# Kernel tuning notes

Measured on AMD Instinct MI355X. Metric: run time of the kernel, lower is better.

The kernel has to match this reference:

```python
import jax, jax.numpy as jnp
import numpy as np

B = 4
IN_DIM = 512
HID = 1024
MLP_LAYERS = 2
SEQ = 4096          # output_dim / sequence_length
RH = 64             # ripl_hidden_dim
RL = 2              # ripl_num_layers
MULT = 1            # ripl_coordinate_multipler

MID_DIM = 2 * RH * RH + (RH + 1) * RH      # per middle ripple layer param count
OUT_DIM = 2 * RH * 1 + (RH + 1) * 1        # output ripple layer param count
MLP_OUT = RL * MID_DIM + OUT_DIM


def gelu(x):
    return jax.nn.gelu(x, approximate=False)


def layer_norm(x, g, b, eps=1e-5):
    mu = jnp.mean(x, axis=-1, keepdims=True)
    var = jnp.var(x, axis=-1, keepdims=True)
    return (x - mu) * jax.lax.rsqrt(var + eps) * g + b


def batch_ripple(x, w, b):
    # x: (B,S,I), w: (B,O,I,2), b: (B,O,I+1)
    # out[b,s,o] = b[b,o,0] + sum_i b[b,o,i+1] * sin(w[b,o,i,0]*x[b,s,i] + w[b,o,i,1])
    arg = w[:, None, :, :, 0] * x[:, :, None, :] + w[:, None, :, :, 1]  # (B,S,O,I)
    return b[:, None, :, 0] + jnp.sum(jnp.sin(arg) * b[:, None, :, 1:], axis=-1)


def setup_inputs() -> dict:
    key = jax.random.key(0)
    ks = jax.random.split(key, 20)
    s = 0.02
    inp = {
        "x": jax.random.normal(ks[0], (B, IN_DIM), jnp.float32),
        "mlp_w0": jax.random.normal(ks[1], (IN_DIM, HID), jnp.float32) * s,
        "mlp_b0": jnp.zeros((HID,), jnp.float32),
        "mlp_w1": jax.random.normal(ks[2], (HID, HID), jnp.float32) * s,
        "mlp_b1": jnp.zeros((HID,), jnp.float32),
        "ln_g1": jnp.ones((HID,), jnp.float32),
        "ln_b1": jnp.zeros((HID,), jnp.float32),
        "mlp_w2": jax.random.normal(ks[3], (HID, HID), jnp.float32) * s,
        "mlp_b2": jnp.zeros((HID,), jnp.float32),
        "ln_g2": jnp.ones((HID,), jnp.float32),
        "ln_b2": jnp.zeros((HID,), jnp.float32),
        "mlp_w3": jax.random.normal(ks[4], (HID, MLP_OUT), jnp.float32) * s,
        "mlp_b3": jnp.zeros((MLP_OUT,), jnp.float32),
        "lc_w": jax.random.normal(ks[5], (1, RH), jnp.float32) * 0.1,
        "lc_b": jax.random.normal(ks[6], (RH,), jnp.float32) * 0.1,
        "byp_w": jax.random.normal(ks[7], (1, 1, 2), jnp.float32),
        "byp_b": jax.random.normal(ks[8], (1, 2), jnp.float32),
    }
    return inp


def reference(x, mlp_w0, mlp_b0, mlp_w1, mlp_b1, ln_g1, ln_b1,
              mlp_w2, mlp_b2, ln_g2, ln_b2, mlp_w3, mlp_b3,
              lc_w, lc_b, byp_w, byp_b):
    # hypernetwork MLP: Linear+GELU, [Linear+LN+GELU]*2, Linear
    h = gelu(x @ mlp_w0 + mlp_b0)
    h = gelu(layer_norm(h @ mlp_w1 + mlp_b1, ln_g1, ln_b1))
    h = gelu(layer_norm(h @ mlp_w2 + mlp_b2, ln_g2, ln_b2))
    mlp_out = h @ mlp_w3 + mlp_b3                      # (B, MLP_OUT)

    # split into RL middle ripple layers then the output layer
    middles = [mlp_out[:, i * MID_DIM:(i + 1) * MID_DIM] for i in range(RL)]
    out_w = mlp_out[:, RL * MID_DIM:RL * MID_DIM + OUT_DIM]

    # line coordinates -> fc layer
    lc = (jnp.arange(SEQ, dtype=jnp.float32) * MULT)[None, :, None]  # (1,S,1)
    lc = jnp.broadcast_to(lc, (x.shape[0], SEQ, 1))
    lc_x = lc @ lc_w + lc_b                                          # (B,S,RH)
    lc_bypass = lc_x

    for mw in middles:
        w = mw[:, :2 * RH * RH].reshape(-1, RH, RH, 2)
        b = mw[:, 2 * RH * RH:].reshape(-1, RH, RH + 1)
        lc_x = gelu(batch_ripple(lc_x, w, b))

    wo = out_w[:, :2 * RH].reshape(-1, 1, RH, 2)
    bo = out_w[:, 2 * RH:].reshape(-1, 1, RH + 1)
    lc_x = batch_ripple(lc_x, wo, bo)                                # (B,S,1)

    # learned RippleLinear(1,1) bypass, broadcast over features then reduced
    byp = byp_b[0, 0] + jnp.sum(
        jnp.sin(byp_w[0, 0, 0] * lc_bypass + byp_w[0, 0, 1]) * byp_b[0, 1],
        axis=-1, keepdims=True)
    lc_x = lc_x + byp
    return jnp.transpose(lc_x, (0, 2, 1))                            # (B,1,S)
```

## Files before the change

### kernel.cpp

```cpp
#include <hip/hip_runtime.h>
#include <math.h>

#define B_      4
#define IN_DIM  512
#define HID     1024
#define SEQ     4096
#define MID_DIM 12352
#define MLP_OUT 24897
#define INV2PI  0.15915494309189535f

#define MLPT_STRIDE 25088

#define OFF_P0    0
#define OFF_P1    32768
#define OFF_P2    49152
#define OFF_H2    65536
#define OFF_MLPT  69632

__device__ __forceinline__ float gelu_exact(float v) {
    return 0.5f * v * (1.0f + erff(v * 0.70710678118654752f));
}

__device__ __forceinline__ float hw_sin_rev(float r) {
    r = r - __builtin_rintf(r);
    return __builtin_amdgcn_sinf(r);
}

__global__ void k_gemm0(const float* __restrict__ x, const float* __restrict__ w0,
                        float* __restrict__ p0) {
    const int cch = blockIdx.x, kc = blockIdx.y;
    const int tid = threadIdx.x;
    __shared__ float xs[256];
    {
        const int b = tid >> 6, k = tid & 63;
        xs[tid] = x[b * IN_DIM + kc * 64 + k];
    }
    __syncthreads();
    const int b = tid >> 6, cl = tid & 63;
    const int c = cch * 64 + cl;
    const float* wp = w0 + (size_t)(kc * 64) * HID + c;
    const float* xp = xs + b * 64;
    float acc = 0.f;
    #pragma unroll 16
    for (int k = 0; k < 64; ++k) acc = fmaf(xp[k], wp[(size_t)k * HID], acc);
    p0[(kc * 4 + b) * HID + c] = acc;
}

__global__ void k_gemm1(const float* __restrict__ p0, const float* __restrict__ b0,
                        const float* __restrict__ w1, float* __restrict__ p1) {
    const int cch = blockIdx.x, kc = blockIdx.y;
    const int tid = threadIdx.x;
    __shared__ float s_h[1024];
    for (int e = tid; e < 1024; e += 256) {
        const int b = e >> 8, kk = e & 255;
        const int kg = kc * 256 + kk;
        float v = b0[kg];
        #pragma unroll
        for (int j = 0; j < 8; ++j) v += p0[(j * 4 + b) * HID + kg];
        s_h[e] = gelu_exact(v);
    }
    __syncthreads();
    const int b = tid >> 6, cl = tid & 63;
    const int c = cch * 64 + cl;
    const float* wp = w1 + (size_t)(kc * 256) * HID + c;
    const float* hp = s_h + b * 256;
    float acc = 0.f;
    #pragma unroll 16
    for (int k = 0; k < 256; ++k) acc = fmaf(hp[k], wp[(size_t)k * HID], acc);
    p1[(kc * 4 + b) * HID + c] = acc;
}

__global__ void k_gemm2(const float* __restrict__ p1, const float* __restrict__ b1,
                        const float* __restrict__ g1, const float* __restrict__ bl1,
                        const float* __restrict__ w2, float* __restrict__ p2) {
    const int cch = blockIdx.x, kc = blockIdx.y;
    const int tid = threadIdx.x;
    __shared__ __align__(16) float vbuf[4096];
    __shared__ float s_h[1024];
    __shared__ float s_red[8];
    for (int e = tid; e < 4096; e += 256) {
        const int b = e >> 10, c = e & 1023;
        float v = b1[c];
        #pragma unroll
        for (int j = 0; j < 4; ++j) v += p1[(j * 4 + b) * HID + c];
        vbuf[e] = v;
    }
    __syncthreads();
    {
        const int b = tid >> 6, lane = tid & 63;
        float s1 = 0.f, s2 = 0.f;
        #pragma unroll
        for (int jj = 0; jj < 16; ++jj) {
            const float v = vbuf[b * 1024 + lane + 64 * jj];
            s1 += v; s2 += v * v;
        }
        #pragma unroll
        for (int m = 1; m < 64; m <<= 1) {
            s1 += __shfl_xor(s1, m, 64);
            s2 += __shfl_xor(s2, m, 64);
        }
        if (lane == 0) {
            const float mu = s1 * (1.0f / HID);
            s_red[b] = mu;
            s_red[4 + b] = rsqrtf(s2 * (1.0f / HID) - mu * mu + 1e-5f);
        }
    }
    __syncthreads();
    for (int e = tid; e < 1024; e += 256) {
        const int b = e >> 8, kk = e & 255;
        const int c = kc * 256 + kk;
        const float v = vbuf[b * 1024 + c];
        s_h[e] = gelu_exact((v - s_red[b]) * s_red[4 + b] * g1[c] + bl1[c]);
    }
    __syncthreads();
    const int b = tid >> 6, cl = tid & 63;
    const int c = cch * 64 + cl;
    const float* wp = w2 + (size_t)(kc * 256) * HID + c;
    const float* hp = s_h + b * 256;
    float acc = 0.f;
    #pragma unroll 16
    for (int k = 0; k < 256; ++k) acc = fmaf(hp[k], wp[(size_t)k * HID], acc);
    p2[(kc * 4 + b) * HID + c] = acc;
}

__global__ void k_lng2(const float* __restrict__ p2, const float* __restrict__ b2,
                       const float* __restrict__ g2, const float* __restrict__ bl2,
                       float* __restrict__ h2) {
    const int b = blockIdx.x, tid = threadIdx.x;
    float v = b2[tid];
    #pragma unroll
    for (int j = 0; j < 4; ++j) v += p2[(j * 4 + b) * HID + tid];
    float s1 = v, s2 = v * v;
    #pragma unroll
    for (int m = 1; m < 64; m <<= 1) {
        s1 += __shfl_xor(s1, m, 64);
        s2 += __shfl_xor(s2, m, 64);
    }
    __shared__ float r1[16], r2[16], s_mu, s_rs;
    const int lane = tid & 63, wid = tid >> 6;
    if (lane == 0) { r1[wid] = s1; r2[wid] = s2; }
    __syncthreads();
    if (tid == 0) {
        float a = 0.f, c = 0.f;
        #pragma unroll
        for (int j = 0; j < 16; ++j) { a += r1[j]; c += r2[j]; }
        const float mu = a * (1.0f / HID);
        s_mu = mu;
        s_rs = rsqrtf(c * (1.0f / HID) - mu * mu + 1e-5f);
    }
    __syncthreads();
    h2[b * HID + tid] = gelu_exact((v - s_mu) * s_rs * g2[tid] + bl2[tid]);
}

__global__ void k_gemm3T(const float* __restrict__ h2, const float* __restrict__ w3,
                         const float* __restrict__ b3, float* __restrict__ mlpT) {
    const int tid = threadIdx.x;
    const int cl = tid & 63;
    const int bu = __builtin_amdgcn_readfirstlane(tid >> 6);
    const int c_raw = blockIdx.x * 64 + cl;
    const bool valid = c_raw < MLP_OUT;
    const int c = valid ? c_raw : (MLP_OUT - 1);
    const float* hp = h2 + bu * HID;
    const float* wp = w3 + c;
    float acc = 0.f;
    #pragma unroll 16
    for (int k = 0; k < 1024; ++k)
        acc = fmaf(hp[k], wp[(size_t)k * MLP_OUT], acc);
    if (!valid) return;
    const float v = acc + b3[c];
    int d; float sc = 1.f;
    if (c < 2 * MID_DIM) {
        const int l = c / MID_DIM;
        const int rel = c - l * MID_DIM;
        if (rel < 8192) {
            const int o = rel >> 7, low = rel & 127;
            d = l * 12416 + (low & 1) * 4096 + (low >> 1) * 64 + o;
            sc = INV2PI;
        } else {
            const int r2 = rel - 8192;
            const int o = r2 / 65, j = r2 % 65;
            d = (j == 0) ? (l * 12416 + 12288 + o)
                         : (l * 12416 + 8192 + (j - 1) * 64 + o);
        }
    } else {
        const int rel = c - 2 * MID_DIM;
        if (rel < 128)       { d = 24832 + (rel & 1) * 64 + (rel >> 1); sc = INV2PI; }
        else if (rel == 128) { d = 24832 + 192; }
        else                 { d = 24832 + 128 + (rel - 129); }
    }
    mlpT[(size_t)bu * MLPT_STRIDE + d] = v * sc;
}

__global__ void __launch_bounds__(256, 2) k_ripple(
        const float* __restrict__ mlpT, const float* __restrict__ lcw,
        const float* __restrict__ lcb, const float* __restrict__ bypw,
        const float* __restrict__ bypb, float* __restrict__ out) {
    const int tid = threadIdx.x;
    const int b = blockIdx.y;
    const int t0 = blockIdx.x * 32;
    const int lane = tid & 63, wid = tid >> 6, tb = wid * 8;

    __shared__ __align__(16) float s_w[12416];
    __shared__ __align__(16) float s_x[2304];
    __shared__ __align__(16) float s_wo[256];
    __shared__ float s_red[32];

    const float* mb = mlpT + (size_t)b * MLPT_STRIDE;

    {
        const float4* src = reinterpret_cast<const float4*>(mb);
        float4* dst = reinterpret_cast<float4*>(s_w);
        for (int e = tid; e < 3104; e += 256) dst[e] = src[e];
        if (tid < 64)
            reinterpret_cast<float4*>(s_wo)[tid] =
                reinterpret_cast<const float4*>(mb + 24832)[tid];
    }
    const float lw = lcw[lane], lb = lcb[lane];
    for (int e = tid; e < 2048; e += 256) {
        const int i = e >> 5, tt = e & 31;
        s_x[i * 36 + tt] = fmaf((float)(t0 + tt), lcw[i], lcb[i]);
    }
    __syncthreads();

    float acc[8];
    for (int layer = 0; layer < 2; ++layer) {
        const float bc = s_w[12288 + lane];
        #pragma unroll
        for (int j = 0; j < 8; ++j) acc[j] = bc;
        for (int i = 0; i < 64; ++i) {
            const float wsv = s_w[i * 64 + lane];
            const float wov = s_w[4096 + i * 64 + lane];
            const float bsv = s_w[8192 + i * 64 + lane];
            const float4 xa = *reinterpret_cast<const float4*>(&s_x[i * 36 + tb]);
            const float4 xb = *reinterpret_cast<const float4*>(&s_x[i * 36 + tb + 4]);
            const float xv[8] = {xa.x, xa.y, xa.z, xa.w, xb.x, xb.y, xb.z, xb.w};
            #pragma unroll
            for (int j = 0; j < 8; ++j) {
                const float r = fmaf(wsv, xv[j], wov);
                acc[j] = fmaf(hw_sin_rev(r), bsv, acc[j]);
            }
        }
        __syncthreads();
        if (layer == 0) {
            #pragma unroll
            for (int j = 0; j < 8; ++j)
                s_x[lane * 36 + tb + j] = gelu_exact(acc[j]);
            const float4* src = reinterpret_cast<const float4*>(mb + 12416);
            float4* dst = reinterpret_cast<float4*>(s_w);
            for (int e = tid; e < 3104; e += 256) dst[e] = src[e];
            __syncthreads();
        }
    }

    {
        const float wsO = s_wo[lane], woO = s_wo[64 + lane], bsO = s_wo[128 + lane];
        const float bcO = s_wo[192];
        const float bw0 = bypw[0] * INV2PI, bw1 = bypw[1] * INV2PI;
        const float bb0 = bypb[0], bb1 = bypb[1];
        #pragma unroll
        for (int j = 0; j < 8; ++j) {
            const int t = t0 + tb + j;
            const float v = gelu_exact(acc[j]);
            float s = hw_sin_rev(fmaf(wsO, v, woO)) * bsO;
            const float xb = fmaf((float)t, lw, lb);
            s = fmaf(hw_sin_rev(fmaf(bw0, xb, bw1)), bb1, s);
            #pragma unroll
            for (int m = 1; m < 64; m <<= 1) s += __shfl_xor(s, m, 64);
            if (lane == 0) s_red[tb + j] = s + bcO + bb0;
        }
    }
    __syncthreads();
    if (tid < 32) out[(size_t)b * SEQ + t0 + tid] = s_red[tid];
}

extern "C" void kernel_launch(void* const* d_in, const int* in_sizes, int n_in,
                              void* d_out, int out_size, void* d_ws, size_t ws_size,
                              hipStream_t stream) {
    const float* x    = (const float*)d_in[0];
    const float* w0   = (const float*)d_in[1];
    const float* b0   = (const float*)d_in[2];
    const float* w1   = (const float*)d_in[3];
    const float* b1   = (const float*)d_in[4];
    const float* g1   = (const float*)d_in[5];
    const float* bl1  = (const float*)d_in[6];
    const float* w2   = (const float*)d_in[7];
    const float* b2   = (const float*)d_in[8];
    const float* g2   = (const float*)d_in[9];
    const float* bl2  = (const float*)d_in[10];
    const float* w3   = (const float*)d_in[11];
    const float* b3   = (const float*)d_in[12];
    const float* lcw  = (const float*)d_in[13];
    const float* lcb  = (const float*)d_in[14];
    const float* bypw = (const float*)d_in[15];
    const float* bypb = (const float*)d_in[16];
    float* out = (float*)d_out;
    float* ws  = (float*)d_ws;

    float* p0   = ws + OFF_P0;
    float* p1   = ws + OFF_P1;
    float* p2   = ws + OFF_P2;
    float* h2   = ws + OFF_H2;
    float* mlpT = ws + OFF_MLPT;

    k_gemm0 <<<dim3(16, 8), 256, 0, stream>>>(x, w0, p0);
    k_gemm1 <<<dim3(16, 4), 256, 0, stream>>>(p0, b0, w1, p1);
    k_gemm2 <<<dim3(16, 4), 256, 0, stream>>>(p1, b1, g1, bl1, w2, p2);
    k_lng2  <<<B_, 1024,    0, stream>>>(p2, b2, g2, bl2, h2);
    k_gemm3T<<<390, 256,    0, stream>>>(h2, w3, b3, mlpT);
    k_ripple<<<dim3(SEQ / 32, B_), 256, 0, stream>>>(mlpT, lcw, lcb, bypw, bypb, out);
}
```

Baseline: 282.4 us.

## Fuse LayerNorm2 into final GEMM with split-K and atomic accumulation

```diff
diff --git a/kernel.cpp b/kernel.cpp
--- a/kernel.cpp
+++ b/kernel.cpp
@@ -14,8 +14,7 @@
 #define OFF_P0    0
 #define OFF_P1    32768
 #define OFF_P2    49152
-#define OFF_H2    65536
-#define OFF_MLPT  69632
+#define OFF_MLPT  65536
 
 __device__ __forceinline__ float gelu_exact(float v) {
     return 0.5f * v * (1.0f + erff(v * 0.70710678118654752f));
@@ -123,51 +122,75 @@
     p2[(kc * 4 + b) * HID + c] = acc;
 }
 
-__global__ void k_lng2(const float* __restrict__ p2, const float* __restrict__ b2,
-                       const float* __restrict__ g2, const float* __restrict__ bl2,
-                       float* __restrict__ h2) {
-    const int b = blockIdx.x, tid = threadIdx.x;
-    float v = b2[tid];
-    #pragma unroll
-    for (int j = 0; j < 4; ++j) v += p2[(j * 4 + b) * HID + tid];
-    float s1 = v, s2 = v * v;
-    #pragma unroll
-    for (int m = 1; m < 64; m <<= 1) {
-        s1 += __shfl_xor(s1, m, 64);
-        s2 += __shfl_xor(s2, m, 64);
-    }
-    __shared__ float r1[16], r2[16], s_mu, s_rs;
-    const int lane = tid & 63, wid = tid >> 6;
-    if (lane == 0) { r1[wid] = s1; r2[wid] = s2; }
-    __syncthreads();
-    if (tid == 0) {
-        float a = 0.f, c = 0.f;
-        #pragma unroll
-        for (int j = 0; j < 16; ++j) { a += r1[j]; c += r2[j]; }
-        const float mu = a * (1.0f / HID);
-        s_mu = mu;
-        s_rs = rsqrtf(c * (1.0f / HID) - mu * mu + 1e-5f);
-    }
-    __syncthreads();
-    h2[b * HID + tid] = gelu_exact((v - s_mu) * s_rs * g2[tid] + bl2[tid]);
-}
-
-__global__ void k_gemm3T(const float* __restrict__ h2, const float* __restrict__ w3,
-                         const float* __restrict__ b3, float* __restrict__ mlpT) {
-    const int tid = threadIdx.x;
-    const int cl = tid & 63;
-    const int bu = __builtin_amdgcn_readfirstlane(tid >> 6);
-    const int c_raw = blockIdx.x * 64 + cl;
+__global__ void k_gemm3T(const float* __restrict__ p2, const float* __restrict__ b2,
+                         const float* __restrict__ g2, const float* __restrict__ bl2,
+                         const float* __restrict__ w3, const float* __restrict__ b3,
+                         float* __restrict__ mlpT) {
+    const int colb = blockIdx.x;
+    const int kc   = blockIdx.y;
+    const int tid  = threadIdx.x;
+    __shared__ __align__(16) float vbuf[4096];
+    __shared__ __align__(16) float s_h[512];
+    __shared__ float s_red[8];
+
+    for (int e = tid; e < 4096; e += 256) {
+        const int b = e >> 10, c = e & 1023;
+        float v = b2[c];
+        #pragma unroll
+        for (int j = 0; j < 4; ++j) v += p2[(j * 4 + b) * HID + c];
+        vbuf[e] = v;
+    }
+    __syncthreads();
+    {
+        const int b = tid >> 6, lane = tid & 63;
+        float s1 = 0.f, s2 = 0.f;
+        #pragma unroll
+        for (int jj = 0; jj < 16; ++jj) {
+            const float v = vbuf[b * 1024 + lane + 64 * jj];
+            s1 += v; s2 += v * v;
+        }
+        #pragma unroll
+        for (int m = 1; m < 64; m <<= 1) {
+            s1 += __shfl_xor(s1, m, 64);
+            s2 += __shfl_xor(s2, m, 64);
+        }
+        if (lane == 0) {
+            const float mu = s1 * (1.0f / HID);
+            s_red[b] = mu;
+            s_red[4 + b] = rsqrtf(s2 * (1.0f / HID) - mu * mu + 1e-5f);
+        }
+    }
+    __syncthreads();
+    for (int e = tid; e < 512; e += 256) {
+        const int b = e >> 7, kk = e & 127;
+        const int c = kc * 128 + kk;
+        const float v = vbuf[b * 1024 + c];
+        s_h[e] = gelu_exact((v - s_red[b]) * s_red[4 + b] * g2[c] + bl2[c]);
+    }
+    __syncthreads();
+
+    const int c_raw = colb * 256 + tid;
     const bool valid = c_raw < MLP_OUT;
     const int c = valid ? c_raw : (MLP_OUT - 1);
-    const float* hp = h2 + bu * HID;
-    const float* wp = w3 + c;
-    float acc = 0.f;
-    #pragma unroll 16
-    for (int k = 0; k < 1024; ++k)
-        acc = fmaf(hp[k], wp[(size_t)k * MLP_OUT], acc);
+    const float* wp = w3 + (size_t)(kc * 128) * MLP_OUT + c;
+    float a0 = 0.f, a1 = 0.f, a2 = 0.f, a3 = 0.f;
+    #pragma unroll 8
+    for (int kk = 0; kk < 128; kk += 4) {
+        const float wv0 = wp[(size_t)(kk + 0) * MLP_OUT];
+        const float wv1 = wp[(size_t)(kk + 1) * MLP_OUT];
+        const float wv2 = wp[(size_t)(kk + 2) * MLP_OUT];
+        const float wv3 = wp[(size_t)(kk + 3) * MLP_OUT];
+        const float4 h0 = *reinterpret_cast<const float4*>(&s_h[kk]);
+        const float4 h1 = *reinterpret_cast<const float4*>(&s_h[128 + kk]);
+        const float4 h2 = *reinterpret_cast<const float4*>(&s_h[256 + kk]);
+        const float4 h3 = *reinterpret_cast<const float4*>(&s_h[384 + kk]);
+        a0 = fmaf(h0.x, wv0, fmaf(h0.y, wv1, fmaf(h0.z, wv2, fmaf(h0.w, wv3, a0))));
+        a1 = fmaf(h1.x, wv0, fmaf(h1.y, wv1, fmaf(h1.z, wv2, fmaf(h1.w, wv3, a1))));
+        a2 = fmaf(h2.x, wv0, fmaf(h2.y, wv1, fmaf(h2.z, wv2, fmaf(h2.w, wv3, a2))));
+        a3 = fmaf(h3.x, wv0, fmaf(h3.y, wv1, fmaf(h3.z, wv2, fmaf(h3.w, wv3, a3))));
+    }
     if (!valid) return;
-    const float v = acc + b3[c];
+
     int d; float sc = 1.f;
     if (c < 2 * MID_DIM) {
         const int l = c / MID_DIM;
@@ -188,7 +211,11 @@
         else if (rel == 128) { d = 24832 + 192; }
         else                 { d = 24832 + 128 + (rel - 129); }
     }
-    mlpT[(size_t)bu * MLPT_STRIDE + d] = v * sc;
+    const float bias = (kc == 0) ? b3[c] : 0.f;
+    atomicAdd(&mlpT[(size_t)0 * MLPT_STRIDE + d], (a0 + bias) * sc);
+    atomicAdd(&mlpT[(size_t)1 * MLPT_STRIDE + d], (a1 + bias) * sc);
+    atomicAdd(&mlpT[(size_t)2 * MLPT_STRIDE + d], (a2 + bias) * sc);
+    atomicAdd(&mlpT[(size_t)3 * MLPT_STRIDE + d], (a3 + bias) * sc);
 }
 
 __global__ void __launch_bounds__(256, 2) k_ripple(
@@ -299,13 +326,12 @@
     float* p0   = ws + OFF_P0;
     float* p1   = ws + OFF_P1;
     float* p2   = ws + OFF_P2;
-    float* h2   = ws + OFF_H2;
     float* mlpT = ws + OFF_MLPT;
 
     k_gemm0 <<<dim3(16, 8), 256, 0, stream>>>(x, w0, p0);
     k_gemm1 <<<dim3(16, 4), 256, 0, stream>>>(p0, b0, w1, p1);
     k_gemm2 <<<dim3(16, 4), 256, 0, stream>>>(p1, b1, g1, bl1, w2, p2);
-    k_lng2  <<<B_, 1024,    0, stream>>>(p2, b2, g2, bl2, h2);
-    k_gemm3T<<<390, 256,    0, stream>>>(h2, w3, b3, mlpT);
+    hipMemsetAsync(mlpT, 0, (size_t)B_ * MLPT_STRIDE * sizeof(float), stream);
+    k_gemm3T<<<dim3(98, 8), 256, 0, stream>>>(p2, b2, g2, bl2, w3, b3, mlpT);
     k_ripple<<<dim3(SEQ / 32, B_), 256, 0, stream>>>(mlpT, lcw, lcb, bypw, bypb, out);
 }
```

After: 310.1 us. 9.8% more time.

## Split final MLP GEMM over K with register prefetch and separate combine kernel

Applied to the files above, without the earlier changes.

```diff
diff --git a/kernel.cpp b/kernel.cpp
--- a/kernel.cpp
+++ b/kernel.cpp
@@ -15,7 +15,8 @@
 #define OFF_P1    32768
 #define OFF_P2    49152
 #define OFF_H2    65536
-#define OFF_MLPT  69632
+#define OFF_P3    69632
+#define OFF_MLPT  467984
 
 __device__ __forceinline__ float gelu_exact(float v) {
     return 0.5f * v * (1.0f + erff(v * 0.70710678118654752f));
@@ -152,22 +153,61 @@
     h2[b * HID + tid] = gelu_exact((v - s_mu) * s_rs * g2[tid] + bl2[tid]);
 }
 
-__global__ void k_gemm3T(const float* __restrict__ h2, const float* __restrict__ w3,
-                         const float* __restrict__ b3, float* __restrict__ mlpT) {
-    const int tid = threadIdx.x;
-    const int cl = tid & 63;
-    const int bu = __builtin_amdgcn_readfirstlane(tid >> 6);
-    const int c_raw = blockIdx.x * 64 + cl;
+__global__ void k_gemm3(const float* __restrict__ h2, const float* __restrict__ w3,
+                        float* __restrict__ p3) {
+    const int colb = blockIdx.x;
+    const int kc   = blockIdx.y;
+    const int tid  = threadIdx.x;
+    const int c_raw = colb * 256 + tid;
     const bool valid = c_raw < MLP_OUT;
     const int c = valid ? c_raw : (MLP_OUT - 1);
-    const float* hp = h2 + bu * HID;
-    const float* wp = w3 + c;
-    float acc = 0.f;
-    #pragma unroll 16
-    for (int k = 0; k < 1024; ++k)
-        acc = fmaf(hp[k], wp[(size_t)k * MLP_OUT], acc);
+    const float* wp = w3 + (size_t)(kc * 256) * MLP_OUT + c;
+    const float* hp = h2 + kc * 256;
+
+    float a0 = 0.f, a1 = 0.f, a2 = 0.f, a3 = 0.f;
+    float wb[16];
+    #pragma unroll
+    for (int j = 0; j < 16; ++j) wb[j] = wp[(size_t)j * MLP_OUT];
+
+    for (int g = 0; g < 15; ++g) {
+        const int k0 = g * 16;
+        float wn[16];
+        #pragma unroll
+        for (int j = 0; j < 16; ++j) wn[j] = wp[(size_t)(k0 + 16 + j) * MLP_OUT];
+        #pragma unroll
+        for (int j = 0; j < 16; ++j) {
+            const int k = k0 + j;
+            a0 = fmaf(hp[k],        wb[j], a0);
+            a1 = fmaf(hp[1024 + k], wb[j], a1);
+            a2 = fmaf(hp[2048 + k], wb[j], a2);
+            a3 = fmaf(hp[3072 + k], wb[j], a3);
+        }
+        #pragma unroll
+        for (int j = 0; j < 16; ++j) wb[j] = wn[j];
+    }
+    #pragma unroll
+    for (int j = 0; j < 16; ++j) {
+        const int k = 240 + j;
+        a0 = fmaf(hp[k],        wb[j], a0);
+        a1 = fmaf(hp[1024 + k], wb[j], a1);
+        a2 = fmaf(hp[2048 + k], wb[j], a2);
+        a3 = fmaf(hp[3072 + k], wb[j], a3);
+    }
     if (!valid) return;
-    const float v = acc + b3[c];
+    p3[(size_t)(kc * 4 + 0) * MLP_OUT + c] = a0;
+    p3[(size_t)(kc * 4 + 1) * MLP_OUT + c] = a1;
+    p3[(size_t)(kc * 4 + 2) * MLP_OUT + c] = a2;
+    p3[(size_t)(kc * 4 + 3) * MLP_OUT + c] = a3;
+}
+
+__global__ void k_comb3T(const float* __restrict__ p3, const float* __restrict__ b3,
+                         float* __restrict__ mlpT) {
+    const int b = blockIdx.y;
+    const int c = blockIdx.x * 256 + threadIdx.x;
+    if (c >= MLP_OUT) return;
+    float v = b3[c];
+    #pragma unroll
+    for (int j = 0; j < 4; ++j) v += p3[(size_t)(j * 4 + b) * MLP_OUT + c];
     int d; float sc = 1.f;
     if (c < 2 * MID_DIM) {
         const int l = c / MID_DIM;
@@ -188,7 +228,7 @@
         else if (rel == 128) { d = 24832 + 192; }
         else                 { d = 24832 + 128 + (rel - 129); }
     }
-    mlpT[(size_t)bu * MLPT_STRIDE + d] = v * sc;
+    mlpT[(size_t)b * MLPT_STRIDE + d] = v * sc;
 }
 
 __global__ void __launch_bounds__(256, 2) k_ripple(
@@ -300,12 +340,14 @@
     float* p1   = ws + OFF_P1;
     float* p2   = ws + OFF_P2;
     float* h2   = ws + OFF_H2;
+    float* p3   = ws + OFF_P3;
     float* mlpT = ws + OFF_MLPT;
 
     k_gemm0 <<<dim3(16, 8), 256, 0, stream>>>(x, w0, p0);
     k_gemm1 <<<dim3(16, 4), 256, 0, stream>>>(p0, b0, w1, p1);
     k_gemm2 <<<dim3(16, 4), 256, 0, stream>>>(p1, b1, g1, bl1, w2, p2);
     k_lng2  <<<B_, 1024,    0, stream>>>(p2, b2, g2, bl2, h2);
-    k_gemm3T<<<390, 256,    0, stream>>>(h2, w3, b3, mlpT);
+    k_gemm3 <<<dim3(98, 4), 256, 0, stream>>>(h2, w3, p3);
+    k_comb3T<<<dim3(98, 4), 256, 0, stream>>>(p3, b3, mlpT);
     k_ripple<<<dim3(SEQ / 32, B_), 256, 0, stream>>>(mlpT, lcw, lcb, bypw, bypb, out);
 }
```

Result: faster. 263.7 us (-6.6%).
